# Optimization experiments

Hardware: AMD Instinct MI355X
Metric: run time of the kernel (lower is better)

Reference implementation:

```python
import jax, jax.numpy as jnp
import numpy as np

D = 64          # d_in
NH = [256, 256] # nn_depth_design
L = 16          # flow_layers
B = 32768       # batch of samples


def _build_masks():
    # Deterministic mask maps: this_min=0, this_max=d_in-1 for all layers
    mh0 = np.arange(NH[0]) % (D - 1)
    mh1 = np.arange(NH[1]) % (D - 1)
    M1 = (mh0[None, :] <= mh1[:, None]).astype(np.float32)  # [nh1, nh0]
    M0s, M2s = [], []
    for l in range(L):
        perm = np.arange(D) if l % 2 == 0 else np.arange(D)[::-1]
        M0s.append((perm[None, :] <= mh0[:, None]).astype(np.float32))  # [nh0, D]
        M2s.append((mh1[None, :] < perm[:, None]).astype(np.float32))  # [D, nh1]
    M0 = np.stack(M0s)                                   # [L, nh0, D]
    M1 = np.broadcast_to(M1, (L,) + M1.shape).copy()     # [L, nh1, nh0]
    M2 = np.stack(M2s)                                   # [L, D, nh1]
    return jnp.asarray(M0), jnp.asarray(M1), jnp.asarray(M2)


def setup_inputs() -> dict:
    key = jax.random.key(0)
    ks = jax.random.split(key, 13)
    u = jax.random.normal(ks[0], (B, D), dtype=jnp.float32)

    def w(k, shape, fan_in):
        return jax.random.uniform(k, shape, jnp.float32, -1.0, 1.0) / np.sqrt(fan_in)

    inp = {"u": u}
    i = 1
    for net in ("loc", "scale"):
        inp[f"{net}_W0"] = w(ks[i], (L, NH[0], D), D); i += 1
        inp[f"{net}_b0"] = w(ks[i], (L, NH[0]), D); i += 1
        inp[f"{net}_W1"] = w(ks[i], (L, NH[1], NH[0]), NH[0]); i += 1
        inp[f"{net}_b1"] = w(ks[i], (L, NH[1]), NH[0]); i += 1
        inp[f"{net}_W2"] = w(ks[i], (L, D, NH[1]), NH[1]); i += 1
        inp[f"{net}_b2"] = w(ks[i], (L, D), NH[1]); i += 1
    M0, M1, M2 = _build_masks()
    inp["M0"], inp["M1"], inp["M2"] = M0, M1, M2
    return inp


def reference(u, loc_W0, loc_b0, loc_W1, loc_b1, loc_W2, loc_b2,
              scale_W0, scale_b0, scale_W1, scale_b1, scale_W2, scale_b2,
              M0, M1, M2):
    def step(y, p):
        (lW0, lb0, lW1, lb1, lW2, lb2,
         sW0, sb0, sW1, sb1, sW2, sb2, m0, m1, m2) = p

        def net(W0, b0, W1, b1, W2, b2):
            h = jax.nn.relu(y @ (m0 * W0).T + b0)    # [B, nh0]
            h = jax.nn.relu(h @ (m1 * W1).T + b1)    # [B, nh1]
            return h @ (m2 * W2).T + b2              # [B, D]

        loc = net(lW0, lb0, lW1, lb1, lW2, lb2)
        sc = net(sW0, sb0, sW1, sb1, sW2, sb2)
        # inverse=False coupling: exp(-scale) * (y - loc)
        return jnp.exp(-sc) * (y - loc), None

    params = (loc_W0, loc_b0, loc_W1, loc_b1, loc_W2, loc_b2,
              scale_W0, scale_b0, scale_W1, scale_b1, scale_W2, scale_b2,
              M0, M1, M2)
    y, _ = jax.lax.scan(step, u, params)
    return y
```

## Files before the change

kernel.cpp:

```cpp
#include <hip/hip_runtime.h>
#include <hip/hip_bf16.h>

typedef __bf16 bf16x8 __attribute__((ext_vector_type(8)));
typedef __bf16 bf16x4 __attribute__((ext_vector_type(4)));
typedef float  f32x4  __attribute__((ext_vector_type(4)));

#define LAYERS 16
#define DIM 64
#define NHID 256
#define BATCH 32768
#define MTILE 64
#define NBLOCKS (BATCH / MTILE)

#define W0P_PER 16384
#define W1P_PER 65536
#define W2P_PER 16384
#define W0P_TOT (32 * W0P_PER)
#define W1P_TOT (32 * W1P_PER)
#define W2P_TOT (32 * W2P_PER)
#define PACK_TOT (W0P_TOT + W1P_TOT + W2P_TOT)

__device__ __forceinline__ bf16x8 ldw(const __bf16* p) { return *(const bf16x8*)p; }

__global__ __launch_bounds__(256) void pack_weights(
    const float* __restrict__ lW0, const float* __restrict__ lW1, const float* __restrict__ lW2,
    const float* __restrict__ sW0, const float* __restrict__ sW1, const float* __restrict__ sW2,
    __bf16* __restrict__ ws)
{
    const long i = ((long)blockIdx.x * 256 + threadIdx.x) * 8;
    const float* W; long src; int l, n, k, which;
    if (i < W0P_TOT) {
        int netl = (int)(i / W0P_PER), rem = (int)(i % W0P_PER);
        int net = netl >> 4; l = netl & 15;
        int nt = rem >> 10, kt = (rem >> 9) & 1, lane = (rem >> 3) & 63;
        n = nt * 16 + (lane & 15); k = kt * 32 + (lane >> 4) * 8;
        W = net ? sW0 : lW0; which = 0;
        src = (long)(l * 256 + n) * 64 + k;
    } else if (i < W0P_TOT + W1P_TOT) {
        long r = i - W0P_TOT;
        int netl = (int)(r / W1P_PER), rem = (int)(r % W1P_PER);
        int net = netl >> 4; l = netl & 15;
        int nt = rem >> 12, kt = (rem >> 9) & 7, lane = (rem >> 3) & 63;
        n = nt * 16 + (lane & 15); k = kt * 32 + (lane >> 4) * 8;
        W = net ? sW1 : lW1; which = 1;
        src = (long)(l * 256 + n) * 256 + k;
    } else {
        long r = i - W0P_TOT - W1P_TOT;
        int netl = (int)(r / W2P_PER), rem = (int)(r % W2P_PER);
        int net = netl >> 4; l = netl & 15;
        int nt = rem >> 12, kt = (rem >> 9) & 7, lane = (rem >> 3) & 63;
        n = nt * 16 + (lane & 15); k = kt * 32 + (lane >> 4) * 8;
        W = net ? sW2 : lW2; which = 2;
        src = (long)(l * 64 + n) * 256 + k;
    }
    f32x4 wa = *(const f32x4*)(W + src);
    f32x4 wb = *(const f32x4*)(W + src + 4);
    const int nm = n % 63;
    const int pn = (l & 1) ? 63 - n : n;
    bf16x8 o;
    #pragma unroll
    for (int j = 0; j < 8; ++j) {
        int kk = k + j;
        bool m;
        if (which == 0)      { int pk = (l & 1) ? 63 - kk : kk; m = (pk <= nm); }
        else if (which == 1) { m = ((kk % 63) <= nm); }
        else                 { m = ((kk % 63) < pn); }
        float v = (j < 4) ? wa[j] : wb[j - 4];
        o[j] = m ? (__bf16)v : (__bf16)0.0f;
    }
    *(bf16x8*)(ws + i) = o;
}

__global__ void __launch_bounds__(256, 2)
flow_kernel(
    const float* __restrict__ u,
    const __bf16* __restrict__ wp,
    const float* __restrict__ lb0, const float* __restrict__ lb1, const float* __restrict__ lb2,
    const float* __restrict__ sb0, const float* __restrict__ sb1, const float* __restrict__ sb2,
    float* __restrict__ out)
{
    __shared__ __bf16 ybf[4 * 2 * 512];
    __shared__ __bf16 buf[4 * 8 * 512];

    const int tid  = threadIdx.x;
    const int wave = tid >> 6;
    const int lane = tid & 63;
    const int quad = lane >> 4;
    const int l16  = lane & 15;
    const int blk  = blockIdx.x;

    const int qh = quad >> 1;
    const int qp = (quad & 1) * 4;

    const __bf16* w0p = wp;
    const __bf16* w1p = wp + W0P_TOT;
    const __bf16* w2p = wp + W0P_TOT + W1P_TOT;

    f32x4 y[4];
    #pragma unroll
    for (int bt = 0; bt < 4; ++bt)
        y[bt] = *(const f32x4*)(u + (long)(blk * MTILE + bt * 16 + l16) * DIM
                                  + wave * 16 + quad * 4);

    const int ktY = wave >> 1;
    const int flY = ((wave & 1) * 2 + qh) * 16 + l16;

    bf16x8 wg1[8];
    #pragma unroll
    for (int ot = 0; ot < 4; ++ot)
        #pragma unroll
        for (int kt = 0; kt < 2; ++kt)
            wg1[ot * 2 + kt] = ldw(w0p + (long)((4 * wave + ot) * 2 + kt) * 512 + lane * 8);

    for (int l = 0; l < LAYERS; ++l) {
        #pragma unroll
        for (int bt = 0; bt < 4; ++bt) {
            bf16x4 v;
            #pragma unroll
            for (int r = 0; r < 4; ++r) v[r] = (__bf16)y[bt][r];
            *(bf16x4*)&ybf[((bt * 2 + ktY) * 64 + flY) * 8 + qp] = v;
        }
        __syncthreads();

        f32x4 locr[4], scr[4];

        #pragma unroll
        for (int net = 0; net < 2; ++net) {
            const __bf16* w1b = w1p + (long)(net * 16 + l) * W1P_PER;
            const __bf16* w2b = w2p + (long)(net * 16 + l) * W2P_PER;
            const __bf16* w0n = w0p + (long)(net == 0 ? 16 + l : l + 1) * W0P_PER;
            const float* b0 = (net ? sb0 : lb0) + l * 256;
            const float* b1 = (net ? sb1 : lb1) + l * 256;
            const float* b2 = (net ? sb2 : lb2) + l * 64;

            bf16x8 wg2a[4];

            {
                f32x4 acc[4][4];
                #pragma unroll
                for (int ot = 0; ot < 4; ++ot)
                    #pragma unroll
                    for (int bt = 0; bt < 4; ++bt)
                        acc[ot][bt] = (f32x4){0.f, 0.f, 0.f, 0.f};
                #pragma unroll
                for (int kt = 0; kt < 2; ++kt) {
                    bf16x8 bv[4];
                    #pragma unroll
                    for (int bt = 0; bt < 4; ++bt)
                        bv[bt] = *(const bf16x8*)&ybf[((bt * 2 + kt) * 64 + lane) * 8];
                    #pragma unroll
                    for (int ot = 0; ot < 4; ++ot)
                        #pragma unroll
                        for (int bt = 0; bt < 4; ++bt)
                            acc[ot][bt] = __builtin_amdgcn_mfma_f32_16x16x32_bf16(wg1[ot * 2 + kt], bv[bt], acc[ot][bt], 0, 0, 0);
                }
                #pragma unroll
                for (int ot = 0; ot < 4; ++ot)
                    wg2a[ot] = ldw(w1b + (long)((4 * wave + ot) * 8 + 0) * 512 + lane * 8);
                #pragma unroll
                for (int ot = 0; ot < 4; ++ot) {
                    f32x4 bias = *(const f32x4*)(b0 + (4 * wave + ot) * 16 + quad * 4);
                    const int kt1 = (4 * wave + ot) >> 1;
                    const int fl  = ((ot & 1) * 2 + qh) * 16 + l16;
                    #pragma unroll
                    for (int bt = 0; bt < 4; ++bt) {
                        bf16x4 v;
                        #pragma unroll
                        for (int r = 0; r < 4; ++r)
                            v[r] = (__bf16)fmaxf(acc[ot][bt][r] + bias[r], 0.f);
                        *(bf16x4*)&buf[((bt * 8 + kt1) * 64 + fl) * 8 + qp] = v;
                    }
                }
            }
            __syncthreads();

            bf16x8 wg3[4];
            bf16x4 hv[4][4];

            {
                f32x4 acc2[4][4];
                #pragma unroll
                for (int ot = 0; ot < 4; ++ot)
                    #pragma unroll
                    for (int bt = 0; bt < 4; ++bt)
                        acc2[ot][bt] = (f32x4){0.f, 0.f, 0.f, 0.f};
                #pragma unroll
                for (int kt = 0; kt < 8; ++kt) {
                    bf16x8 aw[4];
                    #pragma unroll
                    for (int ot = 0; ot < 4; ++ot)
                        aw[ot] = (kt < 1) ? wg2a[ot]
                                          : ldw(w1b + (long)((4 * wave + ot) * 8 + kt) * 512 + lane * 8);
                    bf16x8 bv[4];
                    #pragma unroll
                    for (int bt = 0; bt < 4; ++bt)
                        bv[bt] = *(const bf16x8*)&buf[((bt * 8 + kt) * 64 + lane) * 8];
                    #pragma unroll
                    for (int ot = 0; ot < 4; ++ot)
                        #pragma unroll
                        for (int bt = 0; bt < 4; ++bt)
                            acc2[ot][bt] = __builtin_amdgcn_mfma_f32_16x16x32_bf16(aw[ot], bv[bt], acc2[ot][bt], 0, 0, 0);
                }
                #pragma unroll
                for (int ot = 0; ot < 4; ++ot) {
                    f32x4 bias = *(const f32x4*)(b1 + (4 * wave + ot) * 16 + quad * 4);
                    #pragma unroll
                    for (int bt = 0; bt < 4; ++bt)
                        #pragma unroll
                        for (int r = 0; r < 4; ++r)
                            hv[ot][bt][r] = (__bf16)fmaxf(acc2[ot][bt][r] + bias[r], 0.f);
                }
                #pragma unroll
                for (int kt = 0; kt < 4; ++kt)
                    wg3[kt] = ldw(w2b + (long)(wave * 8 + kt) * 512 + lane * 8);
            }
            __syncthreads();

            #pragma unroll
            for (int ot = 0; ot < 4; ++ot) {
                const int kt1 = (4 * wave + ot) >> 1;
                const int fl  = ((ot & 1) * 2 + qh) * 16 + l16;
                #pragma unroll
                for (int bt = 0; bt < 4; ++bt)
                    *(bf16x4*)&buf[((bt * 8 + kt1) * 64 + fl) * 8 + qp] = hv[ot][bt];
            }
            __syncthreads();

            {
                f32x4 acc[4];
                #pragma unroll
                for (int bt = 0; bt < 4; ++bt)
                    acc[bt] = (f32x4){0.f, 0.f, 0.f, 0.f};
                #pragma unroll
                for (int kt = 0; kt < 8; ++kt) {
                    bf16x8 aw = (kt < 4) ? wg3[kt]
                                         : ldw(w2b + (long)(wave * 8 + kt) * 512 + lane * 8);
                    #pragma unroll
                    for (int bt = 0; bt < 4; ++bt) {
                        bf16x8 bv = *(const bf16x8*)&buf[((bt * 8 + kt) * 64 + lane) * 8];
                        acc[bt] = __builtin_amdgcn_mfma_f32_16x16x32_bf16(aw, bv, acc[bt], 0, 0, 0);
                    }
                }
                #pragma unroll
                for (int ot = 0; ot < 4; ++ot)
                    #pragma unroll
                    for (int kt = 0; kt < 2; ++kt)
                        wg1[ot * 2 + kt] = ldw(w0n + (long)((4 * wave + ot) * 2 + kt) * 512 + lane * 8);
                f32x4 bias = *(const f32x4*)(b2 + wave * 16 + quad * 4);
                if (net == 0) {
                    #pragma unroll
                    for (int bt = 0; bt < 4; ++bt)
                        #pragma unroll
                        for (int r = 0; r < 4; ++r)
                            locr[bt][r] = acc[bt][r] + bias[r];
                } else {
                    #pragma unroll
                    for (int bt = 0; bt < 4; ++bt)
                        #pragma unroll
                        for (int r = 0; r < 4; ++r)
                            scr[bt][r] = acc[bt][r] + bias[r];
                }
            }
            if (net == 0) __syncthreads();
        }

        #pragma unroll
        for (int bt = 0; bt < 4; ++bt)
            #pragma unroll
            for (int r = 0; r < 4; ++r)
                y[bt][r] = __expf(-scr[bt][r]) * (y[bt][r] - locr[bt][r]);
    }

    #pragma unroll
    for (int bt = 0; bt < 4; ++bt)
        *(f32x4*)(out + (long)(blk * MTILE + bt * 16 + l16) * DIM
                      + wave * 16 + quad * 4) = y[bt];
}

extern "C" void kernel_launch(void* const* d_in, const int* in_sizes, int n_in,
                              void* d_out, int out_size, void* d_ws, size_t ws_size,
                              hipStream_t stream) {
    const float* u   = (const float*)d_in[0];
    const float* lW0 = (const float*)d_in[1];
    const float* lb0 = (const float*)d_in[2];
    const float* lW1 = (const float*)d_in[3];
    const float* lb1 = (const float*)d_in[4];
    const float* lW2 = (const float*)d_in[5];
    const float* lb2 = (const float*)d_in[6];
    const float* sW0 = (const float*)d_in[7];
    const float* sb0 = (const float*)d_in[8];
    const float* sW1 = (const float*)d_in[9];
    const float* sb1 = (const float*)d_in[10];
    const float* sW2 = (const float*)d_in[11];
    const float* sb2 = (const float*)d_in[12];

    if (ws_size < (size_t)PACK_TOT * sizeof(__bf16)) return;
    __bf16* ws = (__bf16*)d_ws;

    pack_weights<<<PACK_TOT / 8 / 256, 256, 0, stream>>>(
        lW0, lW1, lW2, sW0, sW1, sW2, ws);
    flow_kernel<<<NBLOCKS, 256, 0, stream>>>(
        u, ws, lb0, lb1, lb2, sb0, sb1, sb2, (float*)d_out);
}
```

Baseline: 329.6 us.

## Run loc and scale networks concurrently with 512-thread blocks

The block grows from 4 to 8 waves, with waves 0-3 computing the loc MLP and waves 4-7 computing the scale MLP at the same time, instead of running the two nets one after the other. The hidden buffer in shared memory doubles so both nets' activations sit side by side. The final layer is split so each wave computes both loc and scale for a slice of output dims and batch rows, then applies the coupling update in place. This removes the serial second pass and roughly halves the barriers per layer. In exchange, LDS use per block rises and the __launch_bounds__(512, 2) hint puts tighter limits on registers per thread.

```diff
diff --git a/kernel.cpp b/kernel.cpp
--- a/kernel.cpp
+++ b/kernel.cpp
@@ -71,7 +71,7 @@
     *(bf16x8*)(ws + i) = o;
 }
 
-__global__ void __launch_bounds__(256, 2)
+__global__ void __launch_bounds__(512, 2)
 flow_kernel(
     const float* __restrict__ u,
     const __bf16* __restrict__ wp,
@@ -80,7 +80,7 @@
     float* __restrict__ out)
 {
     __shared__ __bf16 ybf[4 * 2 * 512];
-    __shared__ __bf16 buf[4 * 8 * 512];
+    __shared__ __bf16 buf[4 * 16 * 512];
 
     const int tid  = threadIdx.x;
     const int wave = tid >> 6;
@@ -92,189 +92,190 @@
     const int qh = quad >> 1;
     const int qp = (quad & 1) * 4;
 
+    const int net12 = wave >> 2;
+    const int lob   = (wave & 3) * 4;
+
+    const int dt  = wave >> 1;
+    const int hb2 = (wave & 1) * 2;
+
     const __bf16* w0p = wp;
     const __bf16* w1p = wp + W0P_TOT;
     const __bf16* w2p = wp + W0P_TOT + W1P_TOT;
 
-    f32x4 y[4];
+    f32x4 y[2];
     #pragma unroll
-    for (int bt = 0; bt < 4; ++bt)
-        y[bt] = *(const f32x4*)(u + (long)(blk * MTILE + bt * 16 + l16) * DIM
-                                  + wave * 16 + quad * 4);
-
-    const int ktY = wave >> 1;
-    const int flY = ((wave & 1) * 2 + qh) * 16 + l16;
+    for (int j = 0; j < 2; ++j)
+        y[j] = *(const f32x4*)(u + (long)(blk * MTILE + (hb2 + j) * 16 + l16) * DIM
+                                 + dt * 16 + quad * 4);
+
+    const int ktY = dt >> 1;
+    const int flY = ((dt & 1) * 2 + qh) * 16 + l16;
 
     bf16x8 wg1[8];
     #pragma unroll
     for (int ot = 0; ot < 4; ++ot)
         #pragma unroll
         for (int kt = 0; kt < 2; ++kt)
-            wg1[ot * 2 + kt] = ldw(w0p + (long)((4 * wave + ot) * 2 + kt) * 512 + lane * 8);
+            wg1[ot * 2 + kt] = ldw(w0p + (long)(net12 * 16) * W0P_PER
+                                       + (long)((lob + ot) * 2 + kt) * 512 + lane * 8);
 
     for (int l = 0; l < LAYERS; ++l) {
         #pragma unroll
-        for (int bt = 0; bt < 4; ++bt) {
+        for (int j = 0; j < 2; ++j) {
             bf16x4 v;
             #pragma unroll
-            for (int r = 0; r < 4; ++r) v[r] = (__bf16)y[bt][r];
-            *(bf16x4*)&ybf[((bt * 2 + ktY) * 64 + flY) * 8 + qp] = v;
+            for (int r = 0; r < 4; ++r) v[r] = (__bf16)y[j][r];
+            *(bf16x4*)&ybf[(((hb2 + j) * 2 + ktY) * 64 + flY) * 8 + qp] = v;
         }
         __syncthreads();
 
-        f32x4 locr[4], scr[4];
-
-        #pragma unroll
-        for (int net = 0; net < 2; ++net) {
-            const __bf16* w1b = w1p + (long)(net * 16 + l) * W1P_PER;
-            const __bf16* w2b = w2p + (long)(net * 16 + l) * W2P_PER;
-            const __bf16* w0n = w0p + (long)(net == 0 ? 16 + l : l + 1) * W0P_PER;
-            const float* b0 = (net ? sb0 : lb0) + l * 256;
-            const float* b1 = (net ? sb1 : lb1) + l * 256;
-            const float* b2 = (net ? sb2 : lb2) + l * 64;
-
-            bf16x8 wg2a[4];
-
-            {
-                f32x4 acc[4][4];
+        const __bf16* w1b = w1p + (long)(net12 * 16 + l) * W1P_PER;
+        const __bf16* w2l = w2p + (long)l * W2P_PER;
+        const __bf16* w2s = w2p + (long)(16 + l) * W2P_PER;
+        const float*  b0  = (net12 ? sb0 : lb0) + l * 256;
+        const float*  b1  = (net12 ? sb1 : lb1) + l * 256;
+
+        bf16x8 wg2a[4];
+
+        {
+            f32x4 acc[4][4];
+            #pragma unroll
+            for (int ot = 0; ot < 4; ++ot)
+                #pragma unroll
+                for (int bt = 0; bt < 4; ++bt)
+                    acc[ot][bt] = (f32x4){0.f, 0.f, 0.f, 0.f};
+            #pragma unroll
+            for (int kt = 0; kt < 2; ++kt) {
+                bf16x8 bv[4];
+                #pragma unroll
+                for (int bt = 0; bt < 4; ++bt)
+                    bv[bt] = *(const bf16x8*)&ybf[((bt * 2 + kt) * 64 + lane) * 8];
                 #pragma unroll
                 for (int ot = 0; ot < 4; ++ot)
                     #pragma unroll
                     for (int bt = 0; bt < 4; ++bt)
-                        acc[ot][bt] = (f32x4){0.f, 0.f, 0.f, 0.f};
-                #pragma unroll
-                for (int kt = 0; kt < 2; ++kt) {
-                    bf16x8 bv[4];
+                        acc[ot][bt] = __builtin_amdgcn_mfma_f32_16x16x32_bf16(wg1[ot * 2 + kt], bv[bt], acc[ot][bt], 0, 0, 0);
+            }
+            #pragma unroll
+            for (int ot = 0; ot < 4; ++ot)
+                wg2a[ot] = ldw(w1b + (long)((lob + ot) * 8) * 512 + lane * 8);
+            #pragma unroll
+            for (int ot = 0; ot < 4; ++ot) {
+                const int o = net12 * 16 + lob + ot;
+                f32x4 bias = *(const f32x4*)(b0 + (lob + ot) * 16 + quad * 4);
+                const int ktf = o >> 1;
+                const int fl  = ((o & 1) * 2 + qh) * 16 + l16;
+                #pragma unroll
+                for (int bt = 0; bt < 4; ++bt) {
+                    bf16x4 v;
                     #pragma unroll
-                    for (int bt = 0; bt < 4; ++bt)
-                        bv[bt] = *(const bf16x8*)&ybf[((bt * 2 + kt) * 64 + lane) * 8];
-                    #pragma unroll
-                    for (int ot = 0; ot < 4; ++ot)
-                        #pragma unroll
-                        for (int bt = 0; bt < 4; ++bt)
-                            acc[ot][bt] = __builtin_amdgcn_mfma_f32_16x16x32_bf16(wg1[ot * 2 + kt], bv[bt], acc[ot][bt], 0, 0, 0);
+                    for (int r = 0; r < 4; ++r)
+                        v[r] = (__bf16)fmaxf(acc[ot][bt][r] + bias[r], 0.f);
+                    *(bf16x4*)&buf[((bt * 16 + ktf) * 64 + fl) * 8 + qp] = v;
                 }
+            }
+        }
+        __syncthreads();
+
+        bf16x8 wg3[4];
+        bf16x4 hv[4][4];
+
+        {
+            f32x4 acc2[4][4];
+            #pragma unroll
+            for (int ot = 0; ot < 4; ++ot)
+                #pragma unroll
+                for (int bt = 0; bt < 4; ++bt)
+                    acc2[ot][bt] = (f32x4){0.f, 0.f, 0.f, 0.f};
+            #pragma unroll
+            for (int kt = 0; kt < 8; ++kt) {
+                bf16x8 aw[4];
                 #pragma unroll
                 for (int ot = 0; ot < 4; ++ot)
-                    wg2a[ot] = ldw(w1b + (long)((4 * wave + ot) * 8 + 0) * 512 + lane * 8);
-                #pragma unroll
-                for (int ot = 0; ot < 4; ++ot) {
-                    f32x4 bias = *(const f32x4*)(b0 + (4 * wave + ot) * 16 + quad * 4);
-                    const int kt1 = (4 * wave + ot) >> 1;
-                    const int fl  = ((ot & 1) * 2 + qh) * 16 + l16;
-                    #pragma unroll
-                    for (int bt = 0; bt < 4; ++bt) {
-                        bf16x4 v;
-                        #pragma unroll
-                        for (int r = 0; r < 4; ++r)
-                            v[r] = (__bf16)fmaxf(acc[ot][bt][r] + bias[r], 0.f);
-                        *(bf16x4*)&buf[((bt * 8 + kt1) * 64 + fl) * 8 + qp] = v;
-                    }
-                }
-            }
-            __syncthreads();
-
-            bf16x8 wg3[4];
-            bf16x4 hv[4][4];
-
-            {
-                f32x4 acc2[4][4];
+                    aw[ot] = (kt < 1) ? wg2a[ot]
+                                      : ldw(w1b + (long)((lob + ot) * 8 + kt) * 512 + lane * 8);
+                bf16x8 bv[4];
+                #pragma unroll
+                for (int bt = 0; bt < 4; ++bt)
+                    bv[bt] = *(const bf16x8*)&buf[((bt * 16 + net12 * 8 + kt) * 64 + lane) * 8];
                 #pragma unroll
                 for (int ot = 0; ot < 4; ++ot)
                     #pragma unroll
                     for (int bt = 0; bt < 4; ++bt)
-                        acc2[ot][bt] = (f32x4){0.f, 0.f, 0.f, 0.f};
-                #pragma unroll
-                for (int kt = 0; kt < 8; ++kt) {
-                    bf16x8 aw[4];
+                        acc2[ot][bt] = __builtin_amdgcn_mfma_f32_16x16x32_bf16(aw[ot], bv[bt], acc2[ot][bt], 0, 0, 0);
+            }
+            #pragma unroll
+            for (int ot = 0; ot < 4; ++ot) {
+                f32x4 bias = *(const f32x4*)(b1 + (lob + ot) * 16 + quad * 4);
+                #pragma unroll
+                for (int bt = 0; bt < 4; ++bt)
                     #pragma unroll
-                    for (int ot = 0; ot < 4; ++ot)
-                        aw[ot] = (kt < 1) ? wg2a[ot]
-                                          : ldw(w1b + (long)((4 * wave + ot) * 8 + kt) * 512 + lane * 8);
-                    bf16x8 bv[4];
-                    #pragma unroll
-                    for (int bt = 0; bt < 4; ++bt)
-                        bv[bt] = *(const bf16x8*)&buf[((bt * 8 + kt) * 64 + lane) * 8];
-                    #pragma unroll
-                    for (int ot = 0; ot < 4; ++ot)
-                        #pragma unroll
-                        for (int bt = 0; bt < 4; ++bt)
-                            acc2[ot][bt] = __builtin_amdgcn_mfma_f32_16x16x32_bf16(aw[ot], bv[bt], acc2[ot][bt], 0, 0, 0);
+                    for (int r = 0; r < 4; ++r)
+                        hv[ot][bt][r] = (__bf16)fmaxf(acc2[ot][bt][r] + bias[r], 0.f);
+            }
+            #pragma unroll
+            for (int kt = 0; kt < 2; ++kt) {
+                wg3[kt]     = ldw(w2l + (long)(dt * 8 + kt) * 512 + lane * 8);
+                wg3[2 + kt] = ldw(w2s + (long)(dt * 8 + kt) * 512 + lane * 8);
+            }
+        }
+        __syncthreads();
+
+        #pragma unroll
+        for (int ot = 0; ot < 4; ++ot) {
+            const int o = net12 * 16 + lob + ot;
+            const int ktf = o >> 1;
+            const int fl  = ((o & 1) * 2 + qh) * 16 + l16;
+            #pragma unroll
+            for (int bt = 0; bt < 4; ++bt)
+                *(bf16x4*)&buf[((bt * 16 + ktf) * 64 + fl) * 8 + qp] = hv[ot][bt];
+        }
+        __syncthreads();
+
+        {
+            f32x4 accL[2], accS[2];
+            #pragma unroll
+            for (int j = 0; j < 2; ++j) {
+                accL[j] = (f32x4){0.f, 0.f, 0.f, 0.f};
+                accS[j] = (f32x4){0.f, 0.f, 0.f, 0.f};
+            }
+            #pragma unroll
+            for (int kt = 0; kt < 8; ++kt) {
+                bf16x8 awL = (kt < 2) ? wg3[kt]
+                                      : ldw(w2l + (long)(dt * 8 + kt) * 512 + lane * 8);
+                bf16x8 awS = (kt < 2) ? wg3[2 + kt]
+                                      : ldw(w2s + (long)(dt * 8 + kt) * 512 + lane * 8);
+                #pragma unroll
+                for (int j = 0; j < 2; ++j) {
+                    bf16x8 bvL = *(const bf16x8*)&buf[(((hb2 + j) * 16 + kt) * 64 + lane) * 8];
+                    bf16x8 bvS = *(const bf16x8*)&buf[(((hb2 + j) * 16 + 8 + kt) * 64 + lane) * 8];
+                    accL[j] = __builtin_amdgcn_mfma_f32_16x16x32_bf16(awL, bvL, accL[j], 0, 0, 0);
+                    accS[j] = __builtin_amdgcn_mfma_f32_16x16x32_bf16(awS, bvS, accS[j], 0, 0, 0);
                 }
-                #pragma unroll
-                for (int ot = 0; ot < 4; ++ot) {
-                    f32x4 bias = *(const f32x4*)(b1 + (4 * wave + ot) * 16 + quad * 4);
-                    #pragma unroll
-                    for (int bt = 0; bt < 4; ++bt)
-                        #pragma unroll
-                        for (int r = 0; r < 4; ++r)
-                            hv[ot][bt][r] = (__bf16)fmaxf(acc2[ot][bt][r] + bias[r], 0.f);
+            }
+            const __bf16* w0n = w0p + (long)(net12 * 16 + ((l + 1) & 15)) * W0P_PER;
+            #pragma unroll
+            for (int ot = 0; ot < 4; ++ot)
+                #pragma unroll
+                for (int kt = 0; kt < 2; ++kt)
+                    wg1[ot * 2 + kt] = ldw(w0n + (long)((lob + ot) * 2 + kt) * 512 + lane * 8);
+            f32x4 biasL = *(const f32x4*)(lb2 + l * 64 + dt * 16 + quad * 4);
+            f32x4 biasS = *(const f32x4*)(sb2 + l * 64 + dt * 16 + quad * 4);
+            #pragma unroll
+            for (int j = 0; j < 2; ++j)
+                #pragma unroll
+                for (int r = 0; r < 4; ++r) {
+                    float loc = accL[j][r] + biasL[r];
+                    float sc  = accS[j][r] + biasS[r];
+                    y[j][r] = __expf(-sc) * (y[j][r] - loc);
                 }
-                #pragma unroll
-                for (int kt = 0; kt < 4; ++kt)
-                    wg3[kt] = ldw(w2b + (long)(wave * 8 + kt) * 512 + lane * 8);
-            }
-            __syncthreads();
-
-            #pragma unroll
-            for (int ot = 0; ot < 4; ++ot) {
-                const int kt1 = (4 * wave + ot) >> 1;
-                const int fl  = ((ot & 1) * 2 + qh) * 16 + l16;
-                #pragma unroll
-                for (int bt = 0; bt < 4; ++bt)
-                    *(bf16x4*)&buf[((bt * 8 + kt1) * 64 + fl) * 8 + qp] = hv[ot][bt];
-            }
-            __syncthreads();
-
-            {
-                f32x4 acc[4];
-                #pragma unroll
-                for (int bt = 0; bt < 4; ++bt)
-                    acc[bt] = (f32x4){0.f, 0.f, 0.f, 0.f};
-                #pragma unroll
-                for (int kt = 0; kt < 8; ++kt) {
-                    bf16x8 aw = (kt < 4) ? wg3[kt]
-                                         : ldw(w2b + (long)(wave * 8 + kt) * 512 + lane * 8);
-                    #pragma unroll
-                    for (int bt = 0; bt < 4; ++bt) {
-                        bf16x8 bv = *(const bf16x8*)&buf[((bt * 8 + kt) * 64 + lane) * 8];
-                        acc[bt] = __builtin_amdgcn_mfma_f32_16x16x32_bf16(aw, bv, acc[bt], 0, 0, 0);
-                    }
-                }
-                #pragma unroll
-                for (int ot = 0; ot < 4; ++ot)
-                    #pragma unroll
-                    for (int kt = 0; kt < 2; ++kt)
-                        wg1[ot * 2 + kt] = ldw(w0n + (long)((4 * wave + ot) * 2 + kt) * 512 + lane * 8);
-                f32x4 bias = *(const f32x4*)(b2 + wave * 16 + quad * 4);
-                if (net == 0) {
-                    #pragma unroll
-                    for (int bt = 0; bt < 4; ++bt)
-                        #pragma unroll
-                        for (int r = 0; r < 4; ++r)
-                            locr[bt][r] = acc[bt][r] + bias[r];
-                } else {
-                    #pragma unroll
-                    for (int bt = 0; bt < 4; ++bt)
-                        #pragma unroll
-                        for (int r = 0; r < 4; ++r)
-                            scr[bt][r] = acc[bt][r] + bias[r];
-                }
-            }
-            if (net == 0) __syncthreads();
-        }
-
-        #pragma unroll
-        for (int bt = 0; bt < 4; ++bt)
-            #pragma unroll
-            for (int r = 0; r < 4; ++r)
-                y[bt][r] = __expf(-scr[bt][r]) * (y[bt][r] - locr[bt][r]);
+        }
     }
 
     #pragma unroll
-    for (int bt = 0; bt < 4; ++bt)
-        *(f32x4*)(out + (long)(blk * MTILE + bt * 16 + l16) * DIM
-                      + wave * 16 + quad * 4) = y[bt];
+    for (int j = 0; j < 2; ++j)
+        *(f32x4*)(out + (long)(blk * MTILE + (hb2 + j) * 16 + l16) * DIM
+                      + dt * 16 + quad * 4) = y[j];
 }
 
 extern "C" void kernel_launch(void* const* d_in, const int* in_sizes, int n_in,
@@ -299,6 +300,6 @@
 
     pack_weights<<<PACK_TOT / 8 / 256, 256, 0, stream>>>(
         lW0, lW1, lW2, sW0, sW1, sW2, ws);
-    flow_kernel<<<NBLOCKS, 256, 0, stream>>>(
+    flow_kernel<<<NBLOCKS, 512, 0, stream>>>(
         u, ws, lb0, lb1, lb2, sb0, sb1, sb2, (float*)d_out);
 }
```

Result: slower. 455.5 us (+38.2%).
